# Optimization experiments

Measured on AMD Instinct MI355X. Metric: run time of the kernel, lower is better.

Reference implementation:

```python
import jax, jax.numpy as jnp
import numpy as np

L_MAX = 3
MP_SCALING = 0.1
E = 640000
N_ATOMS = 20000
K = 32


def setup_inputs() -> dict:
    key = jax.random.key(0)
    k1, k2, k3, k4, k5 = jax.random.split(key, 5)
    sh = jax.random.normal(k1, (E, (L_MAX + 1) ** 2), dtype=jnp.float32)
    radial_basis = jax.random.normal(k2, (E, L_MAX + 1, K), dtype=jnp.float32)
    center_embedding = jax.random.normal(k3, (N_ATOMS, K), dtype=jnp.float32)
    centers = jax.random.randint(k4, (E,), 0, N_ATOMS, dtype=jnp.int32)
    neighbors = jax.random.randint(k5, (E,), 0, N_ATOMS, dtype=jnp.int32)
    return {
        "sh": sh,
        "radial_basis": radial_basis,
        "center_embedding": center_embedding,
        "centers": centers,
        "neighbors": neighbors,
        "n_atoms": N_ATOMS,
    }


def reference(sh, radial_basis, center_embedding, centers, neighbors, n_atoms):
    # Gather neighbor embeddings once: [E, K]
    emb_n = center_embedding[neighbors]
    blocks = []
    off = 0
    for l in range(L_MAX + 1):
        m = 2 * l + 1
        sh_l = sh[:, off:off + m]            # [E, m]
        off += m
        rb_l = radial_basis[:, l, :]          # [E, K]
        # edge-wise product sh * radial * gathered embedding: [E, m, K]
        src = sh_l[:, :, None] * (rb_l * emb_n)[:, None, :]
        # scatter-add over center atoms -> per-atom density [n_atoms, m, K]
        dens_l = jax.ops.segment_sum(src, centers, num_segments=n_atoms)
        blocks.append(dens_l * MP_SCALING)
    # concatenate per-l blocks along the component axis: [n_atoms, sum(2l+1)=16, K]
    return jnp.concatenate(blocks, axis=1)
```

## Files before the change

kernel.cpp:

```cpp
#include <hip/hip_runtime.h>

#define KDIM 32


__global__ void hist_kernel(const int* __restrict__ centers, int* __restrict__ counts, int n) {
    int i = blockIdx.x * blockDim.x + threadIdx.x;
    if (i < n) atomicAdd(&counts[centers[i]], 1);
}

__global__ void scan_kernel(const int* __restrict__ counts, int* __restrict__ offsets,
                            int* __restrict__ cursor, int n) {
    __shared__ int lds[256];
    int t = threadIdx.x;
    int chunk = (n + 255) >> 8;
    int s = t * chunk;
    int e = min(s + chunk, n);
    int sum = 0;
    for (int i = s; i < e; i++) sum += counts[i];
    lds[t] = sum;
    __syncthreads();
    for (int off = 1; off < 256; off <<= 1) {
        int v = (t >= off) ? lds[t - off] : 0;
        __syncthreads();
        lds[t] += v;
        __syncthreads();
    }
    int run = lds[t] - sum;
    for (int i = s; i < e; i++) {
        int c = counts[i];
        offsets[i] = run;
        cursor[i] = run;
        run += c;
    }
    if (t == 255) offsets[n] = run;
}

__global__ void scatter_kernel(const int* __restrict__ centers, int* __restrict__ cursor,
                               int* __restrict__ edge_ids, int n) {
    int i = blockIdx.x * blockDim.x + threadIdx.x;
    if (i < n) {
        int c = centers[i];
        int pos = atomicAdd(&cursor[c], 1);
        edge_ids[pos] = i;
    }
}


__global__ __launch_bounds__(256) void imp_main_kernel(
    const float* __restrict__ sh, const float* __restrict__ rb,
    const float* __restrict__ emb, const int* __restrict__ neighbors,
    const int* __restrict__ offsets, const int* __restrict__ edge_ids,
    float* __restrict__ out, int n_atoms) {
    int wave = (blockIdx.x * blockDim.x + threadIdx.x) >> 6;
    int lane = threadIdx.x & 63;
    if (wave >= n_atoms) return;
    int k = lane & 31;
    int h = lane >> 5;
    bool hb = (h != 0);

    int start = offsets[wave];
    int end   = offsets[wave + 1];

    float a0 = 0.f, a1 = 0.f, a2 = 0.f, a3 = 0.f;
    float a4 = 0.f, a5 = 0.f, a6 = 0.f, a7 = 0.f;

    for (int i = start; i < end; i++) {
        int e = edge_ids[i];
        e = __builtin_amdgcn_readfirstlane(e);
        int nn = neighbors[e];
        nn = __builtin_amdgcn_readfirstlane(nn);

        float embv = emb[(size_t)nn * KDIM + k];

        const float* rbp = rb + (size_t)e * (4 * KDIM);
        float t0 = rbp[0 * KDIM + k] * embv;
        float t1 = rbp[1 * KDIM + k] * embv;
        float t2 = rbp[2 * KDIM + k] * embv;
        float t3 = rbp[3 * KDIM + k] * embv;

        const float4* shp = (const float4*)(sh + (size_t)e * 16);
        float4 s0 = shp[0];
        float4 s1 = shp[1];
        float4 s2 = shp[2];
        float4 s3 = shp[3];

        float ta = hb ? t1 : t0;
        float td = hb ? t3 : t2;

        a0 += (hb ? s0.y : s0.x) * ta;
        a1 += (hb ? s0.w : s0.z) * t1;
        a2 += (hb ? s1.y : s1.x) * t2;
        a3 += (hb ? s1.w : s1.z) * t2;
        a4 += (hb ? s2.y : s2.x) * td;
        a5 += (hb ? s2.w : s2.z) * t3;
        a6 += (hb ? s3.y : s3.x) * t3;
        a7 += (hb ? s3.w : s3.z) * t3;
    }

    const float SCALE = 0.1f;
    float* op = out + (size_t)wave * (16 * KDIM) + k;
    op[(h + 0)  * KDIM] = a0 * SCALE;
    op[(h + 2)  * KDIM] = a1 * SCALE;
    op[(h + 4)  * KDIM] = a2 * SCALE;
    op[(h + 6)  * KDIM] = a3 * SCALE;
    op[(h + 8)  * KDIM] = a4 * SCALE;
    op[(h + 10) * KDIM] = a5 * SCALE;
    op[(h + 12) * KDIM] = a6 * SCALE;
    op[(h + 14) * KDIM] = a7 * SCALE;
}

extern "C" void kernel_launch(void* const* d_in, const int* in_sizes, int n_in,
                              void* d_out, int out_size, void* d_ws, size_t ws_size,
                              hipStream_t stream) {
    const float* sh        = (const float*)d_in[0];
    const float* rb        = (const float*)d_in[1];
    const float* emb       = (const float*)d_in[2];
    const int*   centers   = (const int*)d_in[3];
    const int*   neighbors = (const int*)d_in[4];

    int E = in_sizes[3];
    int N = in_sizes[2] / KDIM;

    float* out = (float*)d_out;

    int* counts   = (int*)d_ws;
    int* offsets  = counts + N;
    int* cursor   = offsets + N + 1;
    int* edge_ids = cursor + N;

    hipMemsetAsync(counts, 0, (size_t)N * sizeof(int), stream);

    hist_kernel<<<(E + 255) / 256, 256, 0, stream>>>(centers, counts, E);
    scan_kernel<<<1, 256, 0, stream>>>(counts, offsets, cursor, N);
    scatter_kernel<<<(E + 255) / 256, 256, 0, stream>>>(centers, cursor, edge_ids, E);

    int waves = N;
    int blocks = (waves * 64 + 255) / 256;
    imp_main_kernel<<<blocks, 256, 0, stream>>>(sh, rb, emb, neighbors, offsets,
                                                edge_ids, out, N);
}
```

Baseline: 671.2 us.

## Pack edge id with neighbor index, unroll gather loop, widen scan

The scatter pass now writes (edge, neighbor) pairs into the CSR record array, so the main kernel no longer does a dependent load of neighbors[e]. The main loop is unrolled by four so several independent gathers are in flight at once. Each half-wave now reads only its contiguous half of the sh row and writes a contiguous block of eight output rows, which changes the output mapping. The single-block scan is widened from 256 to 1024 threads. In exchange the workspace holds an extra 8 bytes per edge and the unrolled loop uses more registers.

```diff
diff --git a/kernel.cpp b/kernel.cpp
--- a/kernel.cpp
+++ b/kernel.cpp
@@ -8,18 +8,19 @@
     if (i < n) atomicAdd(&counts[centers[i]], 1);
 }
 
-__global__ void scan_kernel(const int* __restrict__ counts, int* __restrict__ offsets,
-                            int* __restrict__ cursor, int n) {
-    __shared__ int lds[256];
+__global__ __launch_bounds__(1024) void scan_kernel(const int* __restrict__ counts,
+                                                    int* __restrict__ offsets,
+                                                    int* __restrict__ cursor, int n) {
+    __shared__ int lds[1024];
     int t = threadIdx.x;
-    int chunk = (n + 255) >> 8;
+    int chunk = (n + 1023) >> 10;
     int s = t * chunk;
     int e = min(s + chunk, n);
     int sum = 0;
     for (int i = s; i < e; i++) sum += counts[i];
     lds[t] = sum;
     __syncthreads();
-    for (int off = 1; off < 256; off <<= 1) {
+    for (int off = 1; off < 1024; off <<= 1) {
         int v = (t >= off) ? lds[t - off] : 0;
         __syncthreads();
         lds[t] += v;
@@ -32,25 +33,48 @@
         cursor[i] = run;
         run += c;
     }
-    if (t == 255) offsets[n] = run;
+    if (t == 1023) offsets[n] = run;
 }
 
-__global__ void scatter_kernel(const int* __restrict__ centers, int* __restrict__ cursor,
-                               int* __restrict__ edge_ids, int n) {
+__global__ void scatter_kernel(const int* __restrict__ centers,
+                               const int* __restrict__ neighbors,
+                               int* __restrict__ cursor,
+                               int2* __restrict__ recs, int n) {
     int i = blockIdx.x * blockDim.x + threadIdx.x;
     if (i < n) {
         int c = centers[i];
+        int nn = neighbors[i];
         int pos = atomicAdd(&cursor[c], 1);
-        edge_ids[pos] = i;
+        recs[pos] = make_int2(i, nn);
     }
 }
 
 
+#define EDGE_BODY(EB, RP, SHP)                                            \
+    {                                                                     \
+        float t0 = RP[0 * KDIM + k] * EB;                                 \
+        float t1 = RP[1 * KDIM + k] * EB;                                 \
+        float t2 = RP[2 * KDIM + k] * EB;                                 \
+        float t3 = RP[3 * KDIM + k] * EB;                                 \
+        float4 sA = SHP[0];                                               \
+        float4 sB = SHP[1];                                               \
+        float c0 = hb ? t2 : t0;                                          \
+        float c1 = hb ? t3 : t1;                                          \
+        float c2 = hb ? t3 : t2;                                          \
+        a0 += sA.x * c0;                                                  \
+        a1 += sA.y * c1;                                                  \
+        a2 += sA.z * c1;                                                  \
+        a3 += sA.w * c1;                                                  \
+        a4 += sB.x * c2;                                                  \
+        a5 += sB.y * c2;                                                  \
+        a6 += sB.z * c2;                                                  \
+        a7 += sB.w * c2;                                                  \
+    }
+
 __global__ __launch_bounds__(256) void imp_main_kernel(
     const float* __restrict__ sh, const float* __restrict__ rb,
-    const float* __restrict__ emb, const int* __restrict__ neighbors,
-    const int* __restrict__ offsets, const int* __restrict__ edge_ids,
-    float* __restrict__ out, int n_atoms) {
+    const float* __restrict__ emb, const int2* __restrict__ recs,
+    const int* __restrict__ offsets, float* __restrict__ out, int n_atoms) {
     int wave = (blockIdx.x * blockDim.x + threadIdx.x) >> 6;
     int lane = threadIdx.x & 63;
     if (wave >= n_atoms) return;
@@ -64,49 +88,61 @@
     float a0 = 0.f, a1 = 0.f, a2 = 0.f, a3 = 0.f;
     float a4 = 0.f, a5 = 0.f, a6 = 0.f, a7 = 0.f;
 
-    for (int i = start; i < end; i++) {
-        int e = edge_ids[i];
-        e = __builtin_amdgcn_readfirstlane(e);
-        int nn = neighbors[e];
-        nn = __builtin_amdgcn_readfirstlane(nn);
+    int i = start;
+    for (; i + 4 <= end; i += 4) {
+        int2 r0 = recs[i + 0];
+        int2 r1 = recs[i + 1];
+        int2 r2 = recs[i + 2];
+        int2 r3 = recs[i + 3];
+        int e0 = __builtin_amdgcn_readfirstlane(r0.x);
+        int n0 = __builtin_amdgcn_readfirstlane(r0.y);
+        int e1 = __builtin_amdgcn_readfirstlane(r1.x);
+        int n1 = __builtin_amdgcn_readfirstlane(r1.y);
+        int e2 = __builtin_amdgcn_readfirstlane(r2.x);
+        int n2 = __builtin_amdgcn_readfirstlane(r2.y);
+        int e3 = __builtin_amdgcn_readfirstlane(r3.x);
+        int n3 = __builtin_amdgcn_readfirstlane(r3.y);
 
-        float embv = emb[(size_t)nn * KDIM + k];
+        float eb0 = emb[(size_t)n0 * KDIM + k];
+        float eb1 = emb[(size_t)n1 * KDIM + k];
+        float eb2 = emb[(size_t)n2 * KDIM + k];
+        float eb3 = emb[(size_t)n3 * KDIM + k];
 
-        const float* rbp = rb + (size_t)e * (4 * KDIM);
-        float t0 = rbp[0 * KDIM + k] * embv;
-        float t1 = rbp[1 * KDIM + k] * embv;
-        float t2 = rbp[2 * KDIM + k] * embv;
-        float t3 = rbp[3 * KDIM + k] * embv;
+        const float* rp0 = rb + (size_t)e0 * (4 * KDIM);
+        const float* rp1 = rb + (size_t)e1 * (4 * KDIM);
+        const float* rp2 = rb + (size_t)e2 * (4 * KDIM);
+        const float* rp3 = rb + (size_t)e3 * (4 * KDIM);
 
-        const float4* shp = (const float4*)(sh + (size_t)e * 16);
-        float4 s0 = shp[0];
-        float4 s1 = shp[1];
-        float4 s2 = shp[2];
-        float4 s3 = shp[3];
+        const float4* sp0 = (const float4*)(sh + (size_t)e0 * 16 + 8 * h);
+        const float4* sp1 = (const float4*)(sh + (size_t)e1 * 16 + 8 * h);
+        const float4* sp2 = (const float4*)(sh + (size_t)e2 * 16 + 8 * h);
+        const float4* sp3 = (const float4*)(sh + (size_t)e3 * 16 + 8 * h);
 
-        float ta = hb ? t1 : t0;
-        float td = hb ? t3 : t2;
-
-        a0 += (hb ? s0.y : s0.x) * ta;
-        a1 += (hb ? s0.w : s0.z) * t1;
-        a2 += (hb ? s1.y : s1.x) * t2;
-        a3 += (hb ? s1.w : s1.z) * t2;
-        a4 += (hb ? s2.y : s2.x) * td;
-        a5 += (hb ? s2.w : s2.z) * t3;
-        a6 += (hb ? s3.y : s3.x) * t3;
-        a7 += (hb ? s3.w : s3.z) * t3;
+        EDGE_BODY(eb0, rp0, sp0)
+        EDGE_BODY(eb1, rp1, sp1)
+        EDGE_BODY(eb2, rp2, sp2)
+        EDGE_BODY(eb3, rp3, sp3)
+    }
+    for (; i < end; i++) {
+        int2 r0 = recs[i];
+        int e0 = __builtin_amdgcn_readfirstlane(r0.x);
+        int n0 = __builtin_amdgcn_readfirstlane(r0.y);
+        float eb0 = emb[(size_t)n0 * KDIM + k];
+        const float* rp0 = rb + (size_t)e0 * (4 * KDIM);
+        const float4* sp0 = (const float4*)(sh + (size_t)e0 * 16 + 8 * h);
+        EDGE_BODY(eb0, rp0, sp0)
     }
 
     const float SCALE = 0.1f;
-    float* op = out + (size_t)wave * (16 * KDIM) + k;
-    op[(h + 0)  * KDIM] = a0 * SCALE;
-    op[(h + 2)  * KDIM] = a1 * SCALE;
-    op[(h + 4)  * KDIM] = a2 * SCALE;
-    op[(h + 6)  * KDIM] = a3 * SCALE;
-    op[(h + 8)  * KDIM] = a4 * SCALE;
-    op[(h + 10) * KDIM] = a5 * SCALE;
-    op[(h + 12) * KDIM] = a6 * SCALE;
-    op[(h + 14) * KDIM] = a7 * SCALE;
+    float* op = out + (size_t)wave * (16 * KDIM) + (size_t)(8 * h) * KDIM + k;
+    op[0 * KDIM] = a0 * SCALE;
+    op[1 * KDIM] = a1 * SCALE;
+    op[2 * KDIM] = a2 * SCALE;
+    op[3 * KDIM] = a3 * SCALE;
+    op[4 * KDIM] = a4 * SCALE;
+    op[5 * KDIM] = a5 * SCALE;
+    op[6 * KDIM] = a6 * SCALE;
+    op[7 * KDIM] = a7 * SCALE;
 }
 
 extern "C" void kernel_launch(void* const* d_in, const int* in_sizes, int n_in,
@@ -123,19 +159,17 @@
 
     float* out = (float*)d_out;
 
-    int* counts   = (int*)d_ws;
-    int* offsets  = counts + N;
-    int* cursor   = offsets + N + 1;
-    int* edge_ids = cursor + N;
+    int2* recs    = (int2*)d_ws;
+    int*  counts  = (int*)(recs + E);
+    int*  offsets = counts + N;
+    int*  cursor  = offsets + N + 1;
 
     hipMemsetAsync(counts, 0, (size_t)N * sizeof(int), stream);
 
     hist_kernel<<<(E + 255) / 256, 256, 0, stream>>>(centers, counts, E);
-    scan_kernel<<<1, 256, 0, stream>>>(counts, offsets, cursor, N);
-    scatter_kernel<<<(E + 255) / 256, 256, 0, stream>>>(centers, cursor, edge_ids, E);
+    scan_kernel<<<1, 1024, 0, stream>>>(counts, offsets, cursor, N);
+    scatter_kernel<<<(E + 255) / 256, 256, 0, stream>>>(centers, neighbors, cursor, recs, E);
 
-    int waves = N;
-    int blocks = (waves * 64 + 255) / 256;
-    imp_main_kernel<<<blocks, 256, 0, stream>>>(sh, rb, emb, neighbors, offsets,
-                                                edge_ids, out, N);
+    int blocks = (N * 64 + 255) / 256;
+    imp_main_kernel<<<blocks, 256, 0, stream>>>(sh, rb, emb, recs, offsets, out, N);
 }
```

Measured after the change: 606.2 us. 9.7% less time.
